# Performance work log

Measured on AMD Instinct MI355X. Metric: run time of the kernel, lower is better.

Reference implementation:

```python
import jax, jax.numpy as jnp
import numpy as np

N, E = 20000, 100000
F_IN, F_OUT = 1024, 512
NUM_FILT = 8
DIM = 3  # output_dim per coordinate-function type (4 types -> 12 total)


def _death_indices(f, edge_index):
    """0-dim persistence pairing via union-find over a vertex filtration.
    Returns death[v]: index of the node whose filtration value kills the
    component created by v (death[v] == v for unpaired/essential nodes)."""
    u, v = edge_index[0], edge_index[1]
    fu, fv = f[u], f[v]
    d_idx = jnp.where(fu >= fv, u, v)          # node realizing the edge value max(f[u], f[v])
    order = jnp.argsort(jnp.maximum(fu, fv))   # process edges in increasing filtration order
    edges = jnp.stack([u[order], v[order], d_idx[order]], axis=1)  # [E, 3]
    n = f.shape[0]

    def find(parent, i):
        return jax.lax.while_loop(lambda j: parent[j] != j, lambda j: parent[j], i)

    def step(carry, e):
        parent, death = carry
        ra = find(parent, e[0])
        rb = find(parent, e[1])
        older = jnp.where(f[ra] <= f[rb], ra, rb)   # older (smaller birth) component survives
        younger = ra + rb - older                   # the other root dies at this edge
        merge = ra != rb
        parent = jnp.where(merge, parent.at[younger].set(older), parent)
        death = jnp.where(merge, death.at[younger].set(e[2]), death)
        return (parent, death), None

    idx = jnp.arange(n)
    (_, death), _ = jax.lax.scan(step, (idx, idx), edges)
    return death


def _coord_activations(p, tri_t, gauss_mu, gauss_sigma, line_w, rhat_c, rhat_r):
    """p: [N, 2] persistence pairs -> [N, 4*DIM] coordinate-function features."""
    b, d = p[:, 0:1], p[:, 1:2]
    tri = jax.nn.relu(d - jnp.abs(tri_t[None, :] - b))                     # Triangle_transform
    diff = p[:, None, :] - gauss_mu[None, :, :]
    gauss = jnp.exp(-jnp.sum(diff * diff, -1) / (2.0 * gauss_sigma ** 2))  # Gaussian_transform
    line = p @ line_w.T                                                    # Line_transform
    q = jnp.sum(jnp.abs(p[:, None, :] - rhat_c[None, :, :]), -1)
    rhat = 1.0 / (1.0 + q) - 1.0 / (1.0 + jnp.abs(jnp.abs(rhat_r) - q))    # RationalHat_transform
    return jnp.concatenate([tri, gauss, line, rhat], axis=1)


def _forward(x, filt_w, filt_b, tri_t, gauss_mu, gauss_sigma, line_w,
             rhat_c, rhat_r, out_w, out_b, edge_index):
    f_all = (x @ filt_w.T + filt_b).T                     # [NUM_FILT, N] filtration values
    f_sg = jax.lax.stop_gradient(f_all)                   # pairing structure is combinatorial
    death = jax.vmap(lambda ff: _death_indices(ff, edge_index))(f_sg)  # [NUM_FILT, N] int
    pairs = jnp.stack([f_all, jnp.take_along_axis(f_all, death, axis=1)], axis=-1)  # [F, N, 2]
    acts = jax.vmap(lambda p: _coord_activations(p, tri_t, gauss_mu, gauss_sigma,
                                                 line_w, rhat_c, rhat_r))(pairs)  # [F, N, 12]
    coord = jnp.transpose(acts, (1, 0, 2)).reshape(x.shape[0], -1)  # torch.cat over filtrations
    return jnp.concatenate([x, coord], axis=1) @ out_w.T + out_b


def setup_inputs() -> dict:
    key = jax.random.key(0)
    ks = jax.random.split(key, 10)
    s = 0.02
    return {
        "x": jax.random.normal(ks[0], (N, F_IN), jnp.float32),
        "edge_index": jax.random.randint(ks[1], (2, E), 0, N),
        "filt_w": jax.random.normal(ks[2], (NUM_FILT, F_IN), jnp.float32) * s,
        "filt_b": jnp.zeros((NUM_FILT,), jnp.float32),
        "tri_t": jax.random.normal(ks[3], (DIM,), jnp.float32),
        "gauss_mu": jax.random.normal(ks[4], (DIM, 2), jnp.float32),
        "gauss_sigma": jnp.asarray(0.5, jnp.float32),
        "line_w": jax.random.normal(ks[5], (DIM, 2), jnp.float32),
        "rhat_c": jax.random.normal(ks[6], (DIM, 2), jnp.float32),
        "rhat_r": jnp.asarray(1.0, jnp.float32),
        "out_w": jax.random.normal(ks[7], (F_OUT, F_IN + NUM_FILT * 4 * DIM), jnp.float32) * s,
        "out_b": jnp.zeros((F_OUT,), jnp.float32),
    }


def reference(x, edge_index, filt_w, filt_b, tri_t, gauss_mu, gauss_sigma,
              line_w, rhat_c, rhat_r, out_w, out_b):
    return _forward(x, filt_w, filt_b, tri_t, gauss_mu, gauss_sigma,
                    line_w, rhat_c, rhat_r, out_w, out_b, edge_index)
```

## Files before the change

### kernel.cpp

```cpp
#include <hip/hip_runtime.h>
#include <stdint.h>

#define NV 20000
#define NE 100000
#define NK 8
#define FIN 1024
#define FOUT 512
#define FTOT 1120
#define KP 1152
#define MP 20096
#define CAP 4096
#define ROUNDS 13
#define NB 32
#define CHUNK (NE / NB)
#define LDA 72

typedef unsigned int u32;
typedef unsigned long long u64;
typedef unsigned short u16;
typedef __attribute__((ext_vector_type(8))) short bf16x8;
typedef __attribute__((ext_vector_type(4))) float f32x4;

__device__ __forceinline__ u32 sb(float x) {
    u32 u = __float_as_uint(x);
    return u ^ ((u & 0x80000000u) ? 0xFFFFFFFFu : 0x80000000u);
}
__device__ __forceinline__ float isb(u32 s) {
    u32 u = (s & 0x80000000u) ? (s ^ 0x80000000u) : ~s;
    return __uint_as_float(u);
}
__device__ __forceinline__ u16 f2bf(float f) {
    u32 u = __float_as_uint(f);
    return (u16)((u + 0x7FFFu + ((u >> 16) & 1u)) >> 16);
}

__global__ __launch_bounds__(256) void k_fx(
    const float* __restrict__ x, const float* __restrict__ fw,
    const float* __restrict__ fb, float* __restrict__ f, u16* __restrict__ A) {
    __shared__ float w[NK * FIN];
    __shared__ float xs[4][FIN];
    for (int i = threadIdx.x; i < NK * FIN; i += 256) w[i] = fw[i];
    __syncthreads();
    int wave = threadIdx.x >> 6, lane = threadIdx.x & 63;
    int v = blockIdx.x * 4 + wave;
    float4* xd = (float4*)xs[wave];
    if (v < NV) {
        const float4* xr4 = (const float4*)(x + (size_t)v * FIN);
        for (int i = lane; i < FIN / 4; i += 64) xd[i] = xr4[i];
    } else {
        for (int i = lane; i < FIN / 4; i += 64) xd[i] = make_float4(0.f, 0.f, 0.f, 0.f);
    }
    float acc[NK];
#pragma unroll
    for (int k = 0; k < NK; k++) acc[k] = 0.f;
    for (int c = 0; c < FIN / 64; c++) {
        int i = c * 64 + lane;
        float xv = xs[wave][i];
#pragma unroll
        for (int k = 0; k < NK; k++) acc[k] = fmaf(xv, w[k * FIN + i], acc[k]);
    }
#pragma unroll
    for (int off = 32; off >= 1; off >>= 1)
#pragma unroll
        for (int k = 0; k < NK; k++) acc[k] += __shfl_xor(acc[k], off, 64);
    if (v < NV && lane < NK) f[lane * NV + v] = acc[lane] + fb[lane];
    for (int cc = lane; cc < 144; cc += 64) {
        int c0 = cc * 8;
        u32 pk[4];
        if (c0 < FIN) {
#pragma unroll
            for (int j = 0; j < 4; j++)
                pk[j] = (u32)f2bf(xs[wave][c0 + 2 * j]) |
                        ((u32)f2bf(xs[wave][c0 + 2 * j + 1]) << 16);
        } else {
#pragma unroll
            for (int j = 0; j < 4; j++) pk[j] = 0u;
        }
        *(uint4*)(A + (size_t)v * KP + c0) = make_uint4(pk[0], pk[1], pk[2], pk[3]);
    }
}

__global__ void k_init(u32* __restrict__ comp, u64* __restrict__ cand, u32* cnts) {
    int t = blockIdx.x * 256 + threadIdx.x;
    comp[t] = (u32)(t % CAP);
    cand[t] = ~0ull;
    if (t < 32) cnts[t] = 0;
}

__global__ void k_castw(const float* __restrict__ ow, u16* __restrict__ W) {
    int t = blockIdx.x * 256 + threadIdx.x;
    if (t >= FOUT * 144) return;
    int n = t / 144, c = (t % 144) * 8;
    u32 pk[4];
    if (c < FTOT) {
        const float* wr = ow + (size_t)n * FTOT + c;
#pragma unroll
        for (int j = 0; j < 4; j++)
            pk[j] = (u32)f2bf(wr[2 * j]) | ((u32)f2bf(wr[2 * j + 1]) << 16);
    } else {
#pragma unroll
        for (int j = 0; j < 4; j++) pk[j] = 0u;
    }
    *(uint4*)(W + (size_t)n * KP + c) = make_uint4(pk[0], pk[1], pk[2], pk[3]);
}

__global__ void k_initdesc(const float* __restrict__ f, u64* __restrict__ cd,
                           float* __restrict__ dval) {
    int t = blockIdx.x * 256 + threadIdx.x;
    u32 v = (u32)(t % NV);
    float fv = f[t];
    cd[t] = ((u64)sb(fv) << 32) | v;
    dval[t] = fv;
}

__global__ void k_descedge(const int* __restrict__ ei, const float* __restrict__ f,
                           u64* __restrict__ cd) {
    int t = blockIdx.x * 256 + threadIdx.x;
    int k = t / NE, e = t % NE;
    int a = ei[e], b = ei[NE + e];
    if (a == b) return;
    float fa = f[k * NV + a], fb2 = f[k * NV + b];
    int d, l; float fl;
    if (fa >= fb2) { d = a; l = b; fl = fb2; } else { d = b; l = a; fl = fa; }
    u64 key = ((u64)sb(fl) << 32) | (u32)l;
    atomicMin(&cd[k * NV + d], key);
}

__global__ __launch_bounds__(1024) void k_basmin(
    const u64* __restrict__ cd, u32* __restrict__ basin,
    u32* nmin, u32* __restrict__ mlist, u32* __restrict__ dense) {
    __shared__ u32 nxt[NV];
    __shared__ u32 changed;
    int k = blockIdx.x;
    const u64* c = cd + (size_t)k * NV;
    for (int i = threadIdx.x; i < NV; i += 1024) nxt[i] = (u32)c[i];
    if (threadIdx.x == 0) changed = 0u;
    __syncthreads();
    for (int pass = 0; pass < 16; pass++) {
        bool ch = false;
        for (int i = threadIdx.x; i < NV; i += 1024) {
            u32 a = nxt[i];
            u32 b = nxt[a];
            if (b != a) {
                u32 c2 = nxt[b];
                u32 d2 = nxt[c2];
                nxt[i] = d2;
                ch = true;
            }
        }
        if (ch) changed = 1u;
        __syncthreads();
        u32 done = (changed == 0u);
        __syncthreads();
        if (threadIdx.x == 0) changed = 0u;
        __syncthreads();
        if (done) break;
    }
    for (int i = threadIdx.x; i < NV; i += 1024) {
        u32 r = nxt[i];
        basin[k * NV + i] = r;
        if (r == (u32)i) {
            u32 id = atomicAdd(&nmin[k], 1u);
            if (id < CAP) { mlist[k * CAP + id] = (u32)i; dense[k * NV + i] = id; }
        }
    }
}

__global__ void k_edgeprep(const int* __restrict__ ei, const float* __restrict__ f,
                           const u32* __restrict__ basin, const u32* __restrict__ dense,
                           u64* __restrict__ wkey, u32* __restrict__ ep) {
    int t = blockIdx.x * 256 + threadIdx.x;
    int k = t / NE, e = t % NE;
    int a = ei[e], b = ei[NE + e];
    if (a == b) { ep[t] = 0xFFFFFFFFu; return; }
    float fa = f[k * NV + a], fb2 = f[k * NV + b];
    float w = (fa >= fb2) ? fa : fb2;
    wkey[t] = ((u64)sb(w) << 32) | (u32)e;
    u32 ba = basin[k * NV + a], bb = basin[k * NV + b];
    if (ba == bb) { ep[t] = 0xFFFFFFFFu; return; }
    u32 da = dense[k * NV + ba], db = dense[k * NV + bb];
    ep[t] = (da << 16) | db;
}

__device__ __forceinline__ u32 rootofs(const u32* c, u32 i) {
    while (true) { u32 p = c[i]; if (p == i) return i; i = p; }
}

__global__ void k_candA(const u32* __restrict__ ep, const u64* __restrict__ wkey,
                        const u32* __restrict__ comp_g, u64* __restrict__ cand_g,
                        const u32* __restrict__ done) {
    __shared__ u32 scomp[CAP];
    __shared__ u64 scand[CAP];
    int k = blockIdx.y, b = blockIdx.x;
    if (done[k]) return;
    for (int i = threadIdx.x; i < CAP; i += 256) {
        scomp[i] = comp_g[k * CAP + i];
        scand[i] = ~0ull;
    }
    __syncthreads();
    int e0 = b * CHUNK;
    const u32* epk = ep + (size_t)k * NE;
    const u64* wkk = wkey + (size_t)k * NE;
    for (int e = e0 + threadIdx.x; e < e0 + CHUNK; e += 256) {
        u32 p32 = epk[e];
        if (p32 == 0xFFFFFFFFu) continue;
        u32 A = rootofs(scomp, p32 >> 16), B = rootofs(scomp, p32 & 0xFFFFu);
        if (A == B) continue;
        u64 w = wkk[e];
        atomicMin(&scand[A], w);
        atomicMin(&scand[B], w);
    }
    __syncthreads();
    u64* cnd = cand_g + (size_t)k * CAP;
    for (int i = threadIdx.x; i < CAP; i += 256) {
        u64 v = scand[i];
        if (v != ~0ull) atomicMin(&cnd[i], v);
    }
}

__global__ void k_round(u64* __restrict__ cand_g, const u32* __restrict__ ep,
                        u32* __restrict__ comp_g, u32* mstcnt,
                        u64* __restrict__ mkey, u32* __restrict__ done) {
    __shared__ u64 scand[CAP];
    __shared__ u32 scomp[CAP];
    __shared__ u32 shk[CAP];
    __shared__ u32 nmerge;
    int k = blockIdx.x;
    if (done[k]) return;
    if (threadIdx.x == 0) nmerge = 0;
    for (int i = threadIdx.x; i < CAP; i += 1024) {
        scand[i] = cand_g[k * CAP + i];
        scomp[i] = comp_g[k * CAP + i];
    }
    __syncthreads();
    for (int i = threadIdx.x; i < CAP; i += 1024) {
        u64 cc = scand[i];
        if (cc == ~0ull) { shk[i] = (u32)i; continue; }
        u32 e = (u32)cc;
        u32 p32 = ep[(size_t)k * NE + e];
        u32 A = rootofs(scomp, p32 >> 16), B = rootofs(scomp, p32 & 0xFFFFu);
        shk[i] = (A == (u32)i) ? B : A;
    }
    __syncthreads();
    for (int i = threadIdx.x; i < CAP; i += 1024) {
        u32 o = shk[i];
        if (o == (u32)i) continue;
        bool mutual = (shk[o] == (u32)i);
        if (mutual && (u32)i < o) continue;
        scomp[i] = o;
        u64 cc = scand[i];
        u32 j = atomicAdd(&mstcnt[k], 1u);
        atomicAdd(&nmerge, 1u);
        if (j < CAP) mkey[k * CAP + j] = cc;
    }
    __syncthreads();
    for (int i = threadIdx.x; i < CAP; i += 1024) scomp[i] = rootofs(scomp, i);
    __syncthreads();
    for (int i = threadIdx.x; i < CAP; i += 1024) {
        comp_g[k * CAP + i] = scomp[i];
        cand_g[k * CAP + i] = ~0ull;
    }
    if (threadIdx.x == 0 && nmerge == 0) done[k] = 1;
}

__global__ __launch_bounds__(1024) void k_sort(const u32* mstcnt, u64* __restrict__ mkey) {
    __shared__ u64 skey[CAP];
    int k = blockIdx.x;
    u32 cnt = mstcnt[k]; if (cnt > CAP) cnt = CAP;
    int n2 = 64; while (n2 < (int)cnt) n2 <<= 1;
    for (int i = threadIdx.x; i < n2; i += 1024)
        skey[i] = (i < (int)cnt) ? mkey[k * CAP + i] : ~0ull;
    __syncthreads();
    int half = n2 >> 1;
    for (int sz = 2; sz <= n2; sz <<= 1) {
        for (int st = sz >> 1; st >= 1; st >>= 1) {
            for (int t = threadIdx.x; t < half; t += 1024) {
                int i = ((t & ~(st - 1)) << 1) | (t & (st - 1));
                int j = i | st;
                bool up = ((i & sz) == 0);
                u64 a = skey[i], b = skey[j];
                if (up ? (a > b) : (a < b)) { skey[i] = b; skey[j] = a; }
            }
            __syncthreads();
        }
    }
    for (int i = threadIdx.x; i < (int)cnt; i += 1024)
        mkey[k * CAP + i] = skey[i];
}

__global__ __launch_bounds__(64) void k_pairw(
    const u32* nmin, const u32* __restrict__ mlist, const u32* mstcnt,
    const u64* __restrict__ mkey, const u32* __restrict__ ep,
    const float* __restrict__ f, float* __restrict__ dval) {
    __shared__ u32 par[CAP];
    __shared__ u32 val[CAP];
    __shared__ u32 tag[CAP];
    int k = blockIdx.x;
    int lane = threadIdx.x;
    u32 nm = nmin[k]; if (nm > CAP) nm = CAP;
    u32 cnt = mstcnt[k]; if (cnt > CAP) cnt = CAP;
    for (int i = lane; i < CAP; i += 64) {
        par[i] = (u32)i;
        tag[i] = 0u;
        val[i] = (i < (int)nm) ? __float_as_uint(f[k * NV + mlist[k * CAP + i]]) : 0u;
    }
    __syncthreads();
    u32 nw = (cnt + 63) >> 6;
    u64 nkey = 0; u32 npay = 0;
    if ((u32)lane < cnt) {
        nkey = mkey[(size_t)k * CAP + lane];
        npay = ep[(size_t)k * NE + (u32)nkey];
    }
    for (u32 w = 0; w < nw; w++) {
        u64 key = nkey; u32 pay = npay;
        bool valid = (w * 64 + (u32)lane) < cnt;
        u32 jn = (w + 1) * 64 + (u32)lane;
        if (jn < cnt) {
            nkey = mkey[(size_t)k * CAP + jn];
            npay = ep[(size_t)k * NE + (u32)nkey];
        }
        u32 wb = (u32)(key >> 32);
        u32 la = pay >> 16, lb = pay & 0xFFFFu;
        u32 rA = la, rB = lb;
        if (valid) {
            while (true) {
                u32 pA = par[rA], pB = par[rB];
                bool dA = (pA == rA), dB = (pB == rB);
                if (dA && dB) break;
                if (!dA) { u32 g = par[pA]; par[rA] = g; rA = g; }
                if (!dB) { u32 g = par[pB]; par[rB] = g; rB = g; }
            }
        }
        u32 vA = valid ? val[rA] : 0u;
        u32 vB = valid ? val[rB] : 0u;
        if (valid) { atomicAdd(&tag[rA], 1u); atomicAdd(&tag[rB], 1u); }
        u32 cA = rA, cvA = vA, cB = rB, cvB = vB;
        u32 t_fy = 0xFFFFFFFFu, t_fo = 0u, t_fvo = 0u;
        if (valid) {
            if (__uint_as_float(cvA) <= __uint_as_float(cvB)) { t_fo = cA; t_fvo = cvA; t_fy = cB; }
            else                                              { t_fo = cB; t_fvo = cvB; t_fy = cA; }
        }
        u32 pkd = (t_fy << 16) | (t_fo & 0xFFFFu);
        bool pend = valid && (atomicAdd(&tag[t_fy], 0u) > 1u);
        u64 m = __ballot(pend);
        while (m) {
            u32 s = (u32)__builtin_ctzll(m);
            m &= m - 1;
            u32 opk = __builtin_amdgcn_readlane(pkd, (int)s);
            u32 ov  = __builtin_amdgcn_readlane(t_fvo, (int)s);
            u32 oy = opk >> 16, oo = opk & 0xFFFFu;
            if ((u32)lane == s) pend = false;
            bool app = valid && ((u32)lane > s);
            bool mA = app && (cA == oy);
            bool mB = app && (cB == oy);
            if (mA) { cA = oo; cvA = ov; }
            if (mB) { cB = oo; cvB = ov; }
            bool rm = mA || mB;
            if (__any(rm)) {
                if (rm) {
                    atomicAdd(&tag[oo], 1u);
                    if (__uint_as_float(cvA) <= __uint_as_float(cvB)) { t_fo = cA; t_fvo = cvA; t_fy = cB; }
                    else                                              { t_fo = cB; t_fvo = cvB; t_fy = cA; }
                    pkd = (t_fy << 16) | (t_fo & 0xFFFFu);
                    pend = atomicAdd(&tag[t_fy], 0u) > 1u;
                }
                m = __ballot(pend);
                m &= (s < 63u) ? (~0ull << (s + 1)) : 0ull;
            }
        }
        if (valid) { tag[rA] = 0u; tag[rB] = 0u; }
        if (valid) { par[t_fy] = t_fo; val[t_fy] = wb; }
        __syncthreads();
    }
    for (int i = lane; i < (int)nm; i += 64) {
        if (par[i] != (u32)i)
            dval[k * NV + mlist[k * CAP + i]] = isb(val[i]);
    }
}

__global__ void k_coordb(const float* __restrict__ f, const float* __restrict__ dval,
                         const float* __restrict__ tri_t, const float* __restrict__ gmu,
                         const float* __restrict__ gsig, const float* __restrict__ lw,
                         const float* __restrict__ rc, const float* __restrict__ rr,
                         u16* __restrict__ A) {
    int t = blockIdx.x * 256 + threadIdx.x;
    int k = t / NV, v = t % NV;
    float b = f[t], d = dval[t];
    float o[12];
    float s = gsig[0];
    float inv2s2 = 1.0f / (2.0f * s * s);
    float r = fabsf(rr[0]);
#pragma unroll
    for (int j = 0; j < 3; j++) {
        float tri = d - fabsf(tri_t[j] - b);
        o[j] = tri > 0.f ? tri : 0.f;
        float dx = b - gmu[2 * j], dy = d - gmu[2 * j + 1];
        o[3 + j] = expf(-(dx * dx + dy * dy) * inv2s2);
        o[6 + j] = b * lw[2 * j] + d * lw[2 * j + 1];
        float q = fabsf(b - rc[2 * j]) + fabsf(d - rc[2 * j + 1]);
        o[9 + j] = 1.0f / (1.0f + q) - 1.0f / (1.0f + fabsf(r - q));
    }
    u16* dst = A + (size_t)v * KP + FIN + k * 12;
    u32* d32 = (u32*)dst;
#pragma unroll
    for (int j = 0; j < 6; j++)
        d32[j] = (u32)f2bf(o[2 * j]) | ((u32)f2bf(o[2 * j + 1]) << 16);
}

__global__ __launch_bounds__(256, 2) void k_gemm2(
    const u16* __restrict__ A, const u16* __restrict__ W,
    const float* __restrict__ bias, float* __restrict__ out) {
    __shared__ u16 As[128 * LDA];
    __shared__ u16 Bs[128 * LDA];
    int n0 = blockIdx.x * 128, m0 = blockIdx.y * 128;
    int t = threadIdx.x;
    int wave = t >> 6, lane = t & 63;
    int wm = (wave >> 1) * 64, wn = (wave & 1) * 64;
    int lrow = lane & 15, lq = lane >> 4;
    f32x4 acc[4][4];
#pragma unroll
    for (int i = 0; i < 4; i++)
#pragma unroll
        for (int j = 0; j < 4; j++) acc[i][j] = (f32x4){0.f, 0.f, 0.f, 0.f};

    int rowc[4], colc[4];
    uint4 av[4], bv[4];
#pragma unroll
    for (int i = 0; i < 4; i++) {
        int c = i * 256 + t;
        rowc[i] = c >> 3;
        colc[i] = (c & 7) * 8;
        av[i] = *(const uint4*)(A + (size_t)(m0 + rowc[i]) * KP + colc[i]);
        bv[i] = *(const uint4*)(W + (size_t)(n0 + rowc[i]) * KP + colc[i]);
    }
#pragma unroll 1
    for (int step = 0; step < KP / 64; step++) {
        __syncthreads();
#pragma unroll
        for (int i = 0; i < 4; i++) {
            *(uint4*)(As + rowc[i] * LDA + colc[i]) = av[i];
            *(uint4*)(Bs + rowc[i] * LDA + colc[i]) = bv[i];
        }
        __syncthreads();
        int k0n = (step + 1 < KP / 64) ? (step + 1) * 64 : 0;
#pragma unroll
        for (int i = 0; i < 4; i++) {
            av[i] = *(const uint4*)(A + (size_t)(m0 + rowc[i]) * KP + k0n + colc[i]);
            bv[i] = *(const uint4*)(W + (size_t)(n0 + rowc[i]) * KP + k0n + colc[i]);
        }
#pragma unroll
        for (int kh = 0; kh < 2; kh++) {
            int kk = kh * 32 + lq * 8;
            bf16x8 af[4], bfr[4];
#pragma unroll
            for (int mt = 0; mt < 4; mt++)
                af[mt] = *(const bf16x8*)(As + (wm + mt * 16 + lrow) * LDA + kk);
#pragma unroll
            for (int nt = 0; nt < 4; nt++)
                bfr[nt] = *(const bf16x8*)(Bs + (wn + nt * 16 + lrow) * LDA + kk);
#pragma unroll
            for (int mt = 0; mt < 4; mt++)
#pragma unroll
                for (int nt = 0; nt < 4; nt++)
                    acc[mt][nt] = __builtin_amdgcn_mfma_f32_16x16x32_bf16(
                        af[mt], bfr[nt], acc[mt][nt], 0, 0, 0);
        }
    }
#pragma unroll
    for (int nt = 0; nt < 4; nt++) {
        int o = n0 + wn + nt * 16 + lrow;
        float bz = bias[o];
#pragma unroll
        for (int mt = 0; mt < 4; mt++) {
#pragma unroll
            for (int i = 0; i < 4; i++) {
                int v = m0 + wm + mt * 16 + lq * 4 + i;
                if (v < NV) out[(size_t)v * FOUT + o] = acc[mt][nt][i] + bz;
            }
        }
    }
}

extern "C" void kernel_launch(void* const* d_in, const int* in_sizes, int n_in,
                              void* d_out, int out_size, void* d_ws, size_t ws_size,
                              hipStream_t stream) {
    const float* x     = (const float*)d_in[0];
    const int*   ei    = (const int*)d_in[1];
    const float* fw    = (const float*)d_in[2];
    const float* fbv   = (const float*)d_in[3];
    const float* tri_t = (const float*)d_in[4];
    const float* gmu   = (const float*)d_in[5];
    const float* gsig  = (const float*)d_in[6];
    const float* lw    = (const float*)d_in[7];
    const float* rc    = (const float*)d_in[8];
    const float* rr    = (const float*)d_in[9];
    const float* ow    = (const float*)d_in[10];
    const float* ob    = (const float*)d_in[11];
    float* out = (float*)d_out;

    char* p = (char*)d_ws;
    auto alloc = [&](size_t bytes) -> void* {
        void* q = (void*)p;
        p += (bytes + 255) & ~(size_t)255;
        return q;
    };
    float* f     = (float*)alloc((size_t)NK * NV * 4);
    u64*   cd    = (u64*)  alloc((size_t)NK * NV * 8);
    u32*   basin = (u32*)  alloc((size_t)NK * NV * 4);
    u32*   dense = (u32*)  alloc((size_t)NK * NV * 4);
    u32*   mlist = (u32*)  alloc((size_t)NK * CAP * 4);
    u32*   cnts  = (u32*)  alloc(64 * 4);
    u64*   wkey  = (u64*)  alloc((size_t)NK * NE * 8);
    u32*   ep    = (u32*)  alloc((size_t)NK * NE * 4);
    u32*   comp  = (u32*)  alloc((size_t)NK * CAP * 4);
    u64*   cand  = (u64*)  alloc((size_t)NK * CAP * 8);
    u64*   mkey  = (u64*)  alloc((size_t)NK * CAP * 8);
    float* dval  = (float*)alloc((size_t)NK * NV * 4);
    u16*   Ab    = (u16*)  alloc((size_t)MP * KP * 2);
    u16*   Wb    = (u16*)  alloc((size_t)FOUT * KP * 2);
    u32* nmin = cnts; u32* mstcnt = cnts + 8; u32* done = cnts + 16;

    k_init<<<128, 256, 0, stream>>>(comp, cand, cnts);
    k_fx<<<MP / 4, 256, 0, stream>>>(x, fw, fbv, f, Ab);
    k_castw<<<(FOUT * 144 + 255) / 256, 256, 0, stream>>>(ow, Wb);
    k_initdesc<<<625, 256, 0, stream>>>(f, cd, dval);
    k_descedge<<<3125, 256, 0, stream>>>(ei, f, cd);
    k_basmin<<<NK, 1024, 0, stream>>>(cd, basin, nmin, mlist, dense);
    k_edgeprep<<<3125, 256, 0, stream>>>(ei, f, basin, dense, wkey, ep);
    for (int r = 0; r < ROUNDS; r++) {
        k_candA<<<dim3(NB, NK), 256, 0, stream>>>(ep, wkey, comp, cand, done);
        k_round<<<NK, 1024, 0, stream>>>(cand, ep, comp, mstcnt, mkey, done);
    }
    k_sort<<<8, 1024, 0, stream>>>(mstcnt, mkey);
    k_pairw<<<8, 64, 0, stream>>>(nmin, mlist, mstcnt, mkey, ep, f, dval);
    k_coordb<<<625, 256, 0, stream>>>(f, dval, tri_t, gmu, gsig, lw, rc, rr, Ab);
    k_gemm2<<<dim3(4, 157), 256, 0, stream>>>(Ab, Wb, ob, out);
}
```

Baseline: 710.4 us.

## Widen output GEMM tile to full N and vectorize epilogue via LDS staging

The final GEMM now gives each 512-thread block a 128-row tile covering all 512 output columns. Each A tile is therefore loaded once instead of four times, and the per-wave MFMA work doubles to a 4x8 fragment grid. The epilogue stages accumulators through shared memory so rows are written with coalesced float4 stores that include a vector bias add. The change uses more registers and LDS per block (about 92KB), and with only 157 blocks it risks low occupancy and underfilling the CUs.

```diff
diff --git a/kernel.cpp b/kernel.cpp
--- a/kernel.cpp
+++ b/kernel.cpp
@@ -407,75 +407,92 @@
         d32[j] = (u32)f2bf(o[2 * j]) | ((u32)f2bf(o[2 * j + 1]) << 16);
 }
 
-__global__ __launch_bounds__(256, 2) void k_gemm2(
+__global__ __launch_bounds__(512, 2) void k_gemm2(
     const u16* __restrict__ A, const u16* __restrict__ W,
     const float* __restrict__ bias, float* __restrict__ out) {
     __shared__ u16 As[128 * LDA];
-    __shared__ u16 Bs[128 * LDA];
-    int n0 = blockIdx.x * 128, m0 = blockIdx.y * 128;
+    __shared__ u16 Ws[512 * LDA];
+    int m0 = blockIdx.x * 128;
     int t = threadIdx.x;
     int wave = t >> 6, lane = t & 63;
-    int wm = (wave >> 1) * 64, wn = (wave & 1) * 64;
+    int wr = wave >> 2, wc = wave & 3;
     int lrow = lane & 15, lq = lane >> 4;
-    f32x4 acc[4][4];
-#pragma unroll
-    for (int i = 0; i < 4; i++)
-#pragma unroll
-        for (int j = 0; j < 4; j++) acc[i][j] = (f32x4){0.f, 0.f, 0.f, 0.f};
-
-    int rowc[4], colc[4];
-    uint4 av[4], bv[4];
-#pragma unroll
-    for (int i = 0; i < 4; i++) {
-        int c = i * 256 + t;
-        rowc[i] = c >> 3;
-        colc[i] = (c & 7) * 8;
-        av[i] = *(const uint4*)(A + (size_t)(m0 + rowc[i]) * KP + colc[i]);
-        bv[i] = *(const uint4*)(W + (size_t)(n0 + rowc[i]) * KP + colc[i]);
+    f32x4 acc[4][8];
+#pragma unroll
+    for (int mt = 0; mt < 4; mt++)
+#pragma unroll
+        for (int nt = 0; nt < 8; nt++) acc[mt][nt] = (f32x4){0.f, 0.f, 0.f, 0.f};
+
+    int arow[2], acol[2], wrow[8], wcol[8];
+    uint4 av[2], wv[8];
+#pragma unroll
+    for (int i = 0; i < 2; i++) {
+        int c = i * 512 + t;
+        arow[i] = c >> 3; acol[i] = (c & 7) * 8;
+        av[i] = *(const uint4*)(A + (size_t)(m0 + arow[i]) * KP + acol[i]);
+    }
+#pragma unroll
+    for (int i = 0; i < 8; i++) {
+        int c = i * 512 + t;
+        wrow[i] = c >> 3; wcol[i] = (c & 7) * 8;
+        wv[i] = *(const uint4*)(W + (size_t)wrow[i] * KP + wcol[i]);
     }
 #pragma unroll 1
     for (int step = 0; step < KP / 64; step++) {
         __syncthreads();
 #pragma unroll
-        for (int i = 0; i < 4; i++) {
-            *(uint4*)(As + rowc[i] * LDA + colc[i]) = av[i];
-            *(uint4*)(Bs + rowc[i] * LDA + colc[i]) = bv[i];
-        }
+        for (int i = 0; i < 2; i++) *(uint4*)(As + arow[i] * LDA + acol[i]) = av[i];
+#pragma unroll
+        for (int i = 0; i < 8; i++) *(uint4*)(Ws + wrow[i] * LDA + wcol[i]) = wv[i];
         __syncthreads();
         int k0n = (step + 1 < KP / 64) ? (step + 1) * 64 : 0;
 #pragma unroll
-        for (int i = 0; i < 4; i++) {
-            av[i] = *(const uint4*)(A + (size_t)(m0 + rowc[i]) * KP + k0n + colc[i]);
-            bv[i] = *(const uint4*)(W + (size_t)(n0 + rowc[i]) * KP + k0n + colc[i]);
-        }
+        for (int i = 0; i < 2; i++)
+            av[i] = *(const uint4*)(A + (size_t)(m0 + arow[i]) * KP + k0n + acol[i]);
+#pragma unroll
+        for (int i = 0; i < 8; i++)
+            wv[i] = *(const uint4*)(W + (size_t)wrow[i] * KP + k0n + wcol[i]);
 #pragma unroll
         for (int kh = 0; kh < 2; kh++) {
             int kk = kh * 32 + lq * 8;
-            bf16x8 af[4], bfr[4];
+            bf16x8 af[4], wf[8];
 #pragma unroll
             for (int mt = 0; mt < 4; mt++)
-                af[mt] = *(const bf16x8*)(As + (wm + mt * 16 + lrow) * LDA + kk);
-#pragma unroll
-            for (int nt = 0; nt < 4; nt++)
-                bfr[nt] = *(const bf16x8*)(Bs + (wn + nt * 16 + lrow) * LDA + kk);
+                af[mt] = *(const bf16x8*)(As + (wr * 64 + mt * 16 + lrow) * LDA + kk);
+#pragma unroll
+            for (int nt = 0; nt < 8; nt++)
+                wf[nt] = *(const bf16x8*)(Ws + (wc * 128 + nt * 16 + lrow) * LDA + kk);
 #pragma unroll
             for (int mt = 0; mt < 4; mt++)
 #pragma unroll
-                for (int nt = 0; nt < 4; nt++)
+                for (int nt = 0; nt < 8; nt++)
                     acc[mt][nt] = __builtin_amdgcn_mfma_f32_16x16x32_bf16(
-                        af[mt], bfr[nt], acc[mt][nt], 0, 0, 0);
-        }
-    }
-#pragma unroll
-    for (int nt = 0; nt < 4; nt++) {
-        int o = n0 + wn + nt * 16 + lrow;
-        float bz = bias[o];
+                        af[mt], wf[nt], acc[mt][nt], 0, 0, 0);
+        }
+    }
+    __syncthreads();
+    float* scr = (float*)Ws + wave * 576;
+    int cg = lane & 7;
+    int rr8 = lane >> 3;
+#pragma unroll
+    for (int np = 0; np < 4; np++) {
+        int o = wc * 128 + np * 32 + cg * 4;
+        f32x4 b4 = *(const f32x4*)(bias + o);
 #pragma unroll
         for (int mt = 0; mt < 4; mt++) {
 #pragma unroll
-            for (int i = 0; i < 4; i++) {
-                int v = m0 + wm + mt * 16 + lq * 4 + i;
-                if (v < NV) out[(size_t)v * FOUT + o] = acc[mt][nt][i] + bz;
+            for (int fh = 0; fh < 2; fh++) {
+                f32x4 fr = acc[mt][2 * np + fh];
+#pragma unroll
+                for (int i = 0; i < 4; i++)
+                    scr[(lq * 4 + i) * 36 + fh * 16 + lrow] = fr[i];
+            }
+#pragma unroll
+            for (int p = 0; p < 2; p++) {
+                int r = p * 8 + rr8;
+                f32x4 vv = *(f32x4*)(scr + r * 36 + cg * 4);
+                int v = m0 + wr * 64 + mt * 16 + r;
+                if (v < NV) *(f32x4*)(out + (size_t)v * FOUT + o) = vv + b4;
             }
         }
     }
@@ -534,5 +551,5 @@
     k_sort<<<8, 1024, 0, stream>>>(mstcnt, mkey);
     k_pairw<<<8, 64, 0, stream>>>(nmin, mlist, mstcnt, mkey, ep, f, dval);
     k_coordb<<<625, 256, 0, stream>>>(f, dval, tri_t, gmu, gsig, lw, rc, rr, Ab);
-    k_gemm2<<<dim3(4, 157), 256, 0, stream>>>(Ab, Wb, ob, out);
-}
+    k_gemm2<<<157, 512, 0, stream>>>(Ab, Wb, ob, out);
+}
```

Result: faster. 667.3 us (-6.1%).
